# Performance work log

Hardware: AMD Instinct MI355X
Metric: run time of the kernel (lower is better)

The kernel has to match this reference:

```python
import jax, jax.numpy as jnp
import numpy as np
from jax.ops import segment_sum, segment_max

N, E, DS, DZ = 16384, 262144, 384, 128
H, D, PQ, PV = 12, 16, 4, 8
EPS = 1e-8


def _quat_to_rot(q):
    q = q / jnp.linalg.norm(q, axis=-1, keepdims=True)
    w, x, y, z = q[:, 0], q[:, 1], q[:, 2], q[:, 3]
    R = jnp.stack([
        1 - 2 * (y * y + z * z), 2 * (x * y - w * z), 2 * (x * z + w * y),
        2 * (x * y + w * z), 1 - 2 * (x * x + z * z), 2 * (y * z - w * x),
        2 * (x * z - w * y), 2 * (y * z + w * x), 1 - 2 * (x * x + y * y),
    ], axis=-1).reshape(-1, 3, 3)
    return R


def setup_inputs() -> dict:
    key = jax.random.key(0)
    ks = jax.random.split(key, 20)
    s = jax.random.normal(ks[0], (N, DS), jnp.float32)
    z = jax.random.normal(ks[1], (E, DZ), jnp.float32)
    edge_index = jax.random.randint(ks[2], (E, 2), 0, N, jnp.int64)
    # valid rigid frames: rotation from random unit quaternion + translation
    R = _quat_to_rot(jax.random.normal(ks[3], (N, 4), jnp.float32))
    t = jax.random.normal(ks[4], (N, 3), jnp.float32)
    f = jnp.zeros((N, 4, 4), jnp.float32).at[:, :3, :3].set(R)
    f = f.at[:, :3, 3].set(t).at[:, 3, 3].set(1.0)

    def lin(k, dout, din):
        return jax.random.normal(k, (dout, din), jnp.float32) / np.sqrt(din)

    hc, hpqk, hpv = H * D, H * PQ * 3, H * PV * 3
    s_out_dim = H * (D * 2 + PV * 4)
    params = dict(
        Wq=lin(ks[5], hc, DS), bq=jnp.zeros((hc,), jnp.float32),
        Wk=lin(ks[6], hc, DS), bk=jnp.zeros((hc,), jnp.float32),
        Wv=lin(ks[7], hc, DS), bv=jnp.zeros((hc,), jnp.float32),
        Wb=lin(ks[8], H, DZ), bb=jnp.zeros((H,), jnp.float32),
        Wqp=lin(ks[9], hpqk, DS), bqp=jnp.zeros((hpqk,), jnp.float32),
        Wkp=lin(ks[10], hpqk, DS), bkp=jnp.zeros((hpqk,), jnp.float32),
        Wvp=lin(ks[11], hpv, DS), bvp=jnp.zeros((hpv,), jnp.float32),
        head_weights=jnp.full((H,), 0.541324854612918, jnp.float32),
        Wpair=lin(ks[12], hc, DZ), bpair=jnp.zeros((hc,), jnp.float32),
        Wo=lin(ks[13], DS, s_out_dim), bo=jnp.zeros((DS,), jnp.float32),
    )
    return dict(s=s, z=z, f=f, edge_index=edge_index, **params)


def _ipa(s, z, f, edge_index, Wq, bq, Wk, bk, Wv, bv, Wb, bb,
         Wqp, bqp, Wkp, bkp, Wvp, bvp, head_weights, Wpair, bpair, Wo, bo):
    n = s.shape[0]
    R, t = f[:, :3, :3], f[:, :3, 3]
    idx_i, idx_j = edge_index[:, 0], edge_index[:, 1]

    norm_attn = (3.0 * D) ** 0.5          # (1/(3d))**-0.5 as in source
    norm_bias = 3.0 ** 0.5
    norm_pt = -0.5 * (3.0 * (PQ * 9.0 / 2)) ** 0.5

    q = (s @ Wq.T + bq).reshape(n, H, D)
    k = (s @ Wk.T + bk).reshape(n, H, D)
    v = (s @ Wv.T + bv).reshape(n, H, D)

    def to_global(pts):  # [n,H,P,3] local -> global
        return jnp.einsum('nij,nhpj->nhpi', R, pts) + t[:, None, None, :]

    q_pts = to_global((s @ Wqp.T + bqp).reshape(n, H, PQ, 3))
    k_pts = to_global((s @ Wkp.T + bkp).reshape(n, H, PQ, 3))
    v_pts = to_global((s @ Wvp.T + bvp).reshape(n, H, PV, 3))

    # scalar QK term + learned pair bias, per edge [E,H]
    attn = jnp.einsum('ehd,ehd->eh', q[idx_i], k[idx_j]) * norm_attn
    attn = attn + (z @ Wb.T + bb) * norm_bias
    # point-distance term
    diff = q_pts[idx_i] - k_pts[idx_j]            # [E,H,PQ,3]
    pt_att = (diff ** 2).sum((-1, -2))            # [E,H]
    pt_att = pt_att * (jax.nn.softplus(head_weights) * norm_pt)
    attn = attn + pt_att

    # segment softmax over edges grouped by destination node idx_i
    m = segment_max(attn, idx_i, num_segments=n)          # [N,H]
    ex = jnp.exp(attn - m[idx_i])
    denom = segment_sum(ex, idx_i, num_segments=n)
    a = ex / denom[idx_i]                                  # [E,H]

    o = segment_sum(a[:, :, None] * v[idx_j], idx_i, num_segments=n)  # [N,H,D]
    o = o.reshape(n, H * D)

    o_pts_g = segment_sum(a[:, :, None, None] * v_pts[idx_j], idx_i,
                          num_segments=n)                  # [N,H,PV,3]
    o_pts_g = o_pts_g.reshape(n, H * PV, 3)
    # invert_apply: R^T (p - t)
    o_pts = jnp.einsum('nji,npj->npi', R, o_pts_g - t[:, None, :])
    o_pts_norm = jnp.sqrt((o_pts ** 2).sum(-1) + EPS)      # [N,H*PV]
    o_pts_flat = o_pts.reshape(n, H * PV * 3)

    v_pair = (z @ Wpair.T + bpair).reshape(-1, H, D)       # [E,H,D]
    o_pair = segment_sum(a[:, :, None] * v_pair, idx_i, num_segments=n)
    o_pair = o_pair.reshape(n, H * D)

    o_s = jnp.concatenate([o, o_pts_flat, o_pts_norm, o_pair], axis=-1)
    return o_s @ Wo.T + bo


def reference(s, z, f, edge_index, Wq, bq, Wk, bk, Wv, bv, Wb, bb,
              Wqp, bqp, Wkp, bkp, Wvp, bvp, head_weights, Wpair, bpair, Wo, bo):
    s_out = _ipa(s, z, f, edge_index, Wq, bq, Wk, bk, Wv, bv, Wb, bb,
                 Wqp, bqp, Wkp, bkp, Wvp, bvp, head_weights, Wpair, bpair, Wo, bo)
    return (s_out, z)
```

## Files before the change

### kernel.cpp

```cpp
#include <hip/hip_runtime.h>

#define NNODE 16384
#define NEDGE 262144
#define DS    384
#define DZ    128
#define NH    12
#define HD    16
#define HC    192
#define HPQK  144
#define HPV   288
#define NCAT  1152
#define FEAT  2144
#define SOUT  384

typedef _Float16 f16;
typedef _Float16 f16x8 __attribute__((ext_vector_type(8)));
typedef _Float16 f16x4 __attribute__((ext_vector_type(4)));
typedef _Float16 f16x2 __attribute__((ext_vector_type(2)));
typedef float    f32x4v __attribute__((ext_vector_type(4)));

#define AS3(p) ((__attribute__((address_space(3))) void*)(p))
#define AS1(p) ((const __attribute__((address_space(1))) void*)(p))
#define WAVE_LDS_FENCE() asm volatile("s_waitcnt lgkmcnt(0)" ::: "memory")

__global__ void k_prep(const float* __restrict__ Wq, const float* __restrict__ Wk,
                       const float* __restrict__ Wv, const float* __restrict__ Wqp,
                       const float* __restrict__ Wkp, const float* __restrict__ Wvp,
                       const float* __restrict__ bq, const float* __restrict__ bk,
                       const float* __restrict__ bv, const float* __restrict__ bqp,
                       const float* __restrict__ bkp, const float* __restrict__ bvp,
                       const float* __restrict__ Wb, const float* __restrict__ Wo,
                       const float* __restrict__ Wpair, const float* __restrict__ bpair,
                       const float* __restrict__ hw,
                       f16* __restrict__ Wcat, float* __restrict__ bcat,
                       f16* __restrict__ Wb16, f16* __restrict__ M2,
                       float* __restrict__ gamv)
{
    int t = blockIdx.x * 256 + threadIdx.x;
    const int T0 = NCAT * DS;
    const int T1 = T0 + NCAT;
    const int T2 = T1 + 16 * DZ;
    const int T3 = T2 + SOUT * FEAT;
    const int T4 = T3 + NH;
    if (t < T0) {
        int r = t / DS, c = t - r * DS;
        float v;
        if      (r < 192) v = Wq [(r      ) * DS + c];
        else if (r < 384) v = Wk [(r - 192) * DS + c];
        else if (r < 576) v = Wv [(r - 384) * DS + c];
        else if (r < 720) v = Wqp[(r - 576) * DS + c];
        else if (r < 864) v = Wkp[(r - 720) * DS + c];
        else              v = Wvp[(r - 864) * DS + c];
        Wcat[t] = (f16)v;
    } else if (t < T1) {
        int r = t - T0;
        float v;
        if      (r < 192) v = bq [r];
        else if (r < 384) v = bk [r - 192];
        else if (r < 576) v = bv [r - 384];
        else if (r < 720) v = bqp[r - 576];
        else if (r < 864) v = bkp[r - 720];
        else              v = bvp[r - 864];
        bcat[r] = v;
    } else if (t < T2) {
        int q = t - T1;
        Wb16[q] = (q < NH * DZ) ? (f16)Wb[q] : (f16)0.0f;
    } else if (t < T3) {
        int q = t - T2;
        int r = q / FEAT, c = q - r * FEAT;
        float v = 0.f;
        if (c < 576) {
            v = Wo[r * 768 + c];
        } else if (c < 2112) {
            int h = (c - 576) >> 7, cc = (c - 576) & 127;
            float acc = 0.f;
            #pragma unroll
            for (int d = 0; d < 16; ++d)
                acc += Wo[r * 768 + 576 + h * 16 + d] * Wpair[(h * 16 + d) * DZ + cc];
            v = acc;
        } else if (c < 2124) {
            int h = c - 2112;
            float acc = 0.f;
            #pragma unroll
            for (int d = 0; d < 16; ++d)
                acc += Wo[r * 768 + 576 + h * 16 + d] * bpair[h * 16 + d];
            v = acc;
        }
        M2[q] = (f16)v;
    } else if (t < T4) {
        int h = t - T3;
        gamv[h] = -3.67423461f * log1pf(__expf(hw[h]));
    }
}

__global__ void k_convert_s(const float4* __restrict__ s4, f16* __restrict__ s16)
{
    int t = blockIdx.x * 256 + threadIdx.x;
    float4 v = s4[t];
    f16x4 o = { (f16)v.x, (f16)v.y, (f16)v.z, (f16)v.w };
    *(f16x4*)(s16 + 4 * (size_t)t) = o;
}

__global__ void k_zcopy(const float4* __restrict__ z4, f16* __restrict__ z16,
                        float4* __restrict__ zout4)
{
    int t = blockIdx.x * 256 + threadIdx.x;
    float4 v = z4[t];
    zout4[t] = v;
    f16x4 o = { (f16)v.x, (f16)v.y, (f16)v.z, (f16)v.w };
    *(f16x4*)(z16 + 4 * (size_t)t) = o;
}

__global__ __launch_bounds__(256) void k_zbias(const f16* __restrict__ z16,
                                               const f16* __restrict__ Wb16,
                                               const float* __restrict__ bb,
                                               float* __restrict__ zbias)
{
    const int wv = threadIdx.x >> 6, lane = threadIdx.x & 63;
    const int row0 = (blockIdx.x * 4 + wv) * 64;
    f16x8 bf[4];
    #pragma unroll
    for (int ks = 0; ks < 4; ++ks)
        bf[ks] = *(const f16x8*)(Wb16 + (lane & 15) * DZ + ks * 32 + (lane >> 4) * 8);
    #pragma unroll
    for (int tt = 0; tt < 4; ++tt) {
        int ra = row0 + tt * 16 + (lane & 15);
        f32x4v acc = {};
        #pragma unroll
        for (int ks = 0; ks < 4; ++ks) {
            f16x8 af = *(const f16x8*)(z16 + (size_t)ra * DZ + ks * 32 + (lane >> 4) * 8);
            acc = __builtin_amdgcn_mfma_f32_16x16x32_f16(af, bf[ks], acc, 0, 0, 0);
        }
        int col = lane & 15;
        if (col < NH) {
            #pragma unroll
            for (int r = 0; r < 4; ++r) {
                int row = row0 + tt * 16 + (lane >> 4) * 4 + r;
                zbias[(size_t)row * NH + col] = (acc[r] + bb[col]) * 1.73205081f;
            }
        }
    }
}

__global__ __launch_bounds__(256) void k_gemm(const f16* __restrict__ A, const f16* __restrict__ B,
                                              const float* __restrict__ bias, float* __restrict__ C,
                                              int M, int N, int K)
{
    __shared__ __align__(16) f16 As[128 * 32];
    __shared__ __align__(16) f16 Bs[128 * 32];
    const int tid = threadIdx.x;
    const int wave = tid >> 6, lane = tid & 63;
    const int bm = blockIdx.x, bn = blockIdx.y;
    const int wm = (wave >> 1) * 64, wn = (wave & 1) * 64;
    f32x4v acc[4][4] = {};
    const int srow = wave * 16 + (lane >> 2);
    const int scol = (lane & 3) * 8;
    const f16* gA0 = A + (size_t)(bm * 128 + srow) * K + scol;
    const f16* gA1 = A + (size_t)(bm * 128 + srow + 64) * K + scol;
    const f16* gB0 = B + (size_t)(bn * 128 + srow) * K + scol;
    const f16* gB1 = B + (size_t)(bn * 128 + srow + 64) * K + scol;
    f16* lA0 = As + wave * 512;
    f16* lA1 = As + (wave + 4) * 512;
    f16* lB0 = Bs + wave * 512;
    f16* lB1 = Bs + (wave + 4) * 512;
    const int fr = lane & 15, fc = (lane >> 4) * 8;
    const int nK = K >> 5;
    for (int kk = 0; kk < nK; ++kk) {
        __syncthreads();
        __builtin_amdgcn_global_load_lds(AS1(gA0), AS3(lA0), 16, 0, 0);
        __builtin_amdgcn_global_load_lds(AS1(gA1), AS3(lA1), 16, 0, 0);
        __builtin_amdgcn_global_load_lds(AS1(gB0), AS3(lB0), 16, 0, 0);
        __builtin_amdgcn_global_load_lds(AS1(gB1), AS3(lB1), 16, 0, 0);
        gA0 += 32; gA1 += 32; gB0 += 32; gB1 += 32;
        __syncthreads();
        f16x8 af[4], bf[4];
        #pragma unroll
        for (int mi = 0; mi < 4; ++mi)
            af[mi] = *(const f16x8*)(As + (wm + mi * 16 + fr) * 32 + fc);
        #pragma unroll
        for (int ni = 0; ni < 4; ++ni)
            bf[ni] = *(const f16x8*)(Bs + (wn + ni * 16 + fr) * 32 + fc);
        #pragma unroll
        for (int mi = 0; mi < 4; ++mi)
            #pragma unroll
            for (int ni = 0; ni < 4; ++ni)
                acc[mi][ni] = __builtin_amdgcn_mfma_f32_16x16x32_f16(af[mi], bf[ni], acc[mi][ni], 0, 0, 0);
    }
    const int r0 = bm * 128 + wm + (lane >> 4) * 4;
    const int c0 = bn * 128 + wn + (lane & 15);
    #pragma unroll
    for (int mi = 0; mi < 4; ++mi)
        #pragma unroll
        for (int ni = 0; ni < 4; ++ni) {
            int col = c0 + ni * 16;
            float b = bias[col];
            #pragma unroll
            for (int r = 0; r < 4; ++r) {
                int row = r0 + mi * 16 + r;
                C[(size_t)row * N + col] = acc[mi][ni][r] + b;
            }
        }
}

__global__ __launch_bounds__(256) void k_gemm16(const f16* __restrict__ A, const f16* __restrict__ B,
                                                const float* __restrict__ bias, f16* __restrict__ C,
                                                int M, int N, int K)
{
    __shared__ __align__(16) f16 As[128 * 32];
    __shared__ __align__(16) f16 Bs[128 * 32];
    const int tid = threadIdx.x;
    const int wave = tid >> 6, lane = tid & 63;
    const int bm = blockIdx.x, bn = blockIdx.y;
    const int wm = (wave >> 1) * 64, wn = (wave & 1) * 64;
    f32x4v acc[4][4] = {};
    const int srow = wave * 16 + (lane >> 2);
    const int scol = (lane & 3) * 8;
    const f16* gA0 = A + (size_t)(bm * 128 + srow) * K + scol;
    const f16* gA1 = A + (size_t)(bm * 128 + srow + 64) * K + scol;
    const f16* gB0 = B + (size_t)(bn * 128 + srow) * K + scol;
    const f16* gB1 = B + (size_t)(bn * 128 + srow + 64) * K + scol;
    f16* lA0 = As + wave * 512;
    f16* lA1 = As + (wave + 4) * 512;
    f16* lB0 = Bs + wave * 512;
    f16* lB1 = Bs + (wave + 4) * 512;
    const int fr = lane & 15, fc = (lane >> 4) * 8;
    const int nK = K >> 5;
    for (int kk = 0; kk < nK; ++kk) {
        __syncthreads();
        __builtin_amdgcn_global_load_lds(AS1(gA0), AS3(lA0), 16, 0, 0);
        __builtin_amdgcn_global_load_lds(AS1(gA1), AS3(lA1), 16, 0, 0);
        __builtin_amdgcn_global_load_lds(AS1(gB0), AS3(lB0), 16, 0, 0);
        __builtin_amdgcn_global_load_lds(AS1(gB1), AS3(lB1), 16, 0, 0);
        gA0 += 32; gA1 += 32; gB0 += 32; gB1 += 32;
        __syncthreads();
        f16x8 af[4], bf[4];
        #pragma unroll
        for (int mi = 0; mi < 4; ++mi)
            af[mi] = *(const f16x8*)(As + (wm + mi * 16 + fr) * 32 + fc);
        #pragma unroll
        for (int ni = 0; ni < 4; ++ni)
            bf[ni] = *(const f16x8*)(Bs + (wn + ni * 16 + fr) * 32 + fc);
        #pragma unroll
        for (int mi = 0; mi < 4; ++mi)
            #pragma unroll
            for (int ni = 0; ni < 4; ++ni)
                acc[mi][ni] = __builtin_amdgcn_mfma_f32_16x16x32_f16(af[mi], bf[ni], acc[mi][ni], 0, 0, 0);
    }
    const int r0 = bm * 128 + wm + (lane >> 4) * 4;
    const int c0 = bn * 128 + wn + (lane & 15);
    #pragma unroll
    for (int mi = 0; mi < 4; ++mi)
        #pragma unroll
        for (int ni = 0; ni < 4; ++ni) {
            int col = c0 + ni * 16;
            float b = bias[col];
            #pragma unroll
            for (int r = 0; r < 4; ++r) {
                int row = r0 + mi * 16 + r;
                C[(size_t)row * N + col] = (f16)(acc[mi][ni][r] + b);
            }
        }
}

__global__ __launch_bounds__(64) void k_nodepost(const f16* __restrict__ raw, const float* __restrict__ fmat,
        f16* __restrict__ Q16, f16* __restrict__ K16, f16* __restrict__ V16,
        f16* __restrict__ QP16, f16* __restrict__ KP16, f16* __restrict__ VP16)
{
    int n = blockIdx.x, l = threadIdx.x;
    const f16* r = raw + (size_t)n * NCAT;
    #pragma unroll
    for (int q = 0; q < 3; ++q) {
        int c = q * 64 + l;
        Q16[(size_t)n * HC + c] = r[c];
        K16[(size_t)n * HC + c] = r[HC + c];
        V16[(size_t)n * HC + c] = r[2 * HC + c];
    }
    const float* fp = fmat + (size_t)n * 16;
    float R00 = fp[0], R01 = fp[1], R02 = fp[2],  t0 = fp[3];
    float R10 = fp[4], R11 = fp[5], R12 = fp[6],  t1 = fp[7];
    float R20 = fp[8], R21 = fp[9], R22 = fp[10], t2 = fp[11];
    if (l < 48) {
        const f16* p = r + 576 + 3 * l;
        float x = (float)p[0], y = (float)p[1], zz = (float)p[2];
        QP16[(size_t)n * HPQK + 3 * l + 0] = (f16)(R00 * x + R01 * y + R02 * zz + t0);
        QP16[(size_t)n * HPQK + 3 * l + 1] = (f16)(R10 * x + R11 * y + R12 * zz + t1);
        QP16[(size_t)n * HPQK + 3 * l + 2] = (f16)(R20 * x + R21 * y + R22 * zz + t2);
        const f16* p2 = r + 720 + 3 * l;
        float x2 = (float)p2[0], y2 = (float)p2[1], z2 = (float)p2[2];
        KP16[(size_t)n * HPQK + 3 * l + 0] = (f16)(R00 * x2 + R01 * y2 + R02 * z2 + t0);
        KP16[(size_t)n * HPQK + 3 * l + 1] = (f16)(R10 * x2 + R11 * y2 + R12 * z2 + t1);
        KP16[(size_t)n * HPQK + 3 * l + 2] = (f16)(R20 * x2 + R21 * y2 + R22 * z2 + t2);
    }
    {
        const f16* p = r + 864 + 3 * l;
        float x = (float)p[0], y = (float)p[1], zz = (float)p[2];
        VP16[(size_t)n * HPV + 3 * l + 0] = (f16)(R00 * x + R01 * y + R02 * zz + t0);
        VP16[(size_t)n * HPV + 3 * l + 1] = (f16)(R10 * x + R11 * y + R12 * zz + t1);
        VP16[(size_t)n * HPV + 3 * l + 2] = (f16)(R20 * x + R21 * y + R22 * zz + t2);
    }
    if (l < 32) {
        int tt = 64 + l;
        const f16* p = r + 864 + 3 * tt;
        float x = (float)p[0], y = (float)p[1], zz = (float)p[2];
        VP16[(size_t)n * HPV + 3 * tt + 0] = (f16)(R00 * x + R01 * y + R02 * zz + t0);
        VP16[(size_t)n * HPV + 3 * tt + 1] = (f16)(R10 * x + R11 * y + R12 * zz + t1);
        VP16[(size_t)n * HPV + 3 * tt + 2] = (f16)(R20 * x + R21 * y + R22 * zz + t2);
    }
}

__global__ void k_zero(int* counts, int* cursor) {
    int t = blockIdx.x * 256 + threadIdx.x;
    if (t < NNODE) counts[t] = 0;
    else if (t < 2 * NNODE) cursor[t - NNODE] = 0;
}
__global__ void k_count(const int* __restrict__ ei, int* counts) {
    int e = blockIdx.x * 256 + threadIdx.x;
    if (e < NEDGE) atomicAdd(&counts[ei[2 * e]], 1);
}
__global__ void k_scan(const int* __restrict__ counts, int* __restrict__ rowptr) {
    __shared__ int lds[256];
    int t = threadIdx.x;
    const int per = NNODE / 256;
    int s = 0;
    for (int i = 0; i < per; ++i) s += counts[t * per + i];
    lds[t] = s; __syncthreads();
    for (int off = 1; off < 256; off <<= 1) {
        int v = (t >= off) ? lds[t - off] : 0;
        __syncthreads();
        lds[t] += v;
        __syncthreads();
    }
    int run = (t == 0) ? 0 : lds[t - 1];
    for (int i = 0; i < per; ++i) { rowptr[t * per + i] = run; run += counts[t * per + i]; }
    if (t == 255) rowptr[NNODE] = run;
}
__global__ void k_scatter(const int* __restrict__ ei, const int* __restrict__ rowptr,
                          int* cursor, int* __restrict__ eids, int* __restrict__ jsorted,
                          int* __restrict__ isorted) {
    int e = blockIdx.x * 256 + threadIdx.x;
    if (e < NEDGE) {
        int i = ei[2 * e];
        int pos = rowptr[i] + atomicAdd(&cursor[i], 1);
        eids[pos] = e;
        jsorted[pos] = ei[2 * e + 1];
        isorted[pos] = i;
    }
}

__global__ __launch_bounds__(256) void k_logits2(
    const int* __restrict__ eids,
    const int* __restrict__ isorted, const int* __restrict__ jsorted,
    const float* __restrict__ zbias,
    const f16* __restrict__ Q16, const f16* __restrict__ K16,
    const f16* __restrict__ QP16, const f16* __restrict__ KP16,
    const float* __restrict__ gamv, float* __restrict__ attn)
{
    const int pos = blockIdx.x * 256 + threadIdx.x;
    const int i = isorted[pos], j = jsorted[pos];
    const int e = eids[pos];
    const f16x8* qr = (const f16x8*)(Q16 + (size_t)i * HC);
    const f16x8* kr = (const f16x8*)(K16 + (size_t)j * HC);
    const f16* qpp = QP16 + (size_t)i * HPQK;
    const f16* kpp = KP16 + (size_t)j * HPQK;
    const float4* zbp = (const float4*)(zbias + (size_t)e * NH);
    float4 zb0 = zbp[0], zb1 = zbp[1], zb2 = zbp[2];
    float zb[NH] = { zb0.x, zb0.y, zb0.z, zb0.w, zb1.x, zb1.y, zb1.z, zb1.w,
                     zb2.x, zb2.y, zb2.z, zb2.w };
    float out[NH];
    #pragma unroll
    for (int h = 0; h < NH; ++h) {
        f16x8 q0 = qr[2 * h], q1 = qr[2 * h + 1];
        f16x8 k0 = kr[2 * h], k1 = kr[2 * h + 1];
        float d = 0.f;
        #pragma unroll
        for (int u = 0; u < 8; ++u)
            d += (float)q0[u] * (float)k0[u] + (float)q1[u] * (float)k1[u];
        float pt = 0.f;
        #pragma unroll
        for (int c = 0; c < 3; ++c) {
            f16x4 qpc = *(const f16x4*)(qpp + 12 * h + 4 * c);
            f16x4 kpc = *(const f16x4*)(kpp + 12 * h + 4 * c);
            #pragma unroll
            for (int u = 0; u < 4; ++u) {
                float dd = (float)qpc[u] - (float)kpc[u];
                pt += dd * dd;
            }
        }
        out[h] = 6.92820323f * d + zb[h] + gamv[h] * pt;
    }
    float4* ao = (float4*)(attn + (size_t)pos * NH);
    ao[0] = make_float4(out[0], out[1], out[2], out[3]);
    ao[1] = make_float4(out[4], out[5], out[6], out[7]);
    ao[2] = make_float4(out[8], out[9], out[10], out[11]);
}

__global__ __launch_bounds__(256) void k_soft(
    const int* __restrict__ rowptr, const float* __restrict__ attn,
    f16* __restrict__ a16, f16* __restrict__ feat)
{
    const int lane = threadIdx.x & 63, wv = threadIdx.x >> 6;
    const int slot = lane >> 4, el = lane & 15;
    const int n = blockIdx.x * 16 + wv * 4 + slot;
    const int base = rowptr[n], deg = rowptr[n + 1] - base;

    f16* fo = feat + (size_t)n * FEAT;
    fo[2112 + el]      = (f16)((el < NH && deg > 0) ? 1.0f : 0.0f);
    fo[2112 + 16 + el] = (f16)0.0f;

    float lg[NH];
    if (deg <= 16) {
        if (el < deg) {
            const float4* ar = (const float4*)(attn + (size_t)(base + el) * NH);
            float4 a0 = ar[0], a1 = ar[1], a2 = ar[2];
            lg[0]=a0.x; lg[1]=a0.y; lg[2]=a0.z; lg[3]=a0.w;
            lg[4]=a1.x; lg[5]=a1.y; lg[6]=a1.z; lg[7]=a1.w;
            lg[8]=a2.x; lg[9]=a2.y; lg[10]=a2.z; lg[11]=a2.w;
        } else {
            #pragma unroll
            for (int h = 0; h < NH; ++h) lg[h] = -1e30f;
        }
        #pragma unroll
        for (int h = 0; h < NH; ++h) {
            float v = lg[h];
            v = fmaxf(v, __shfl_xor(v, 1));
            v = fmaxf(v, __shfl_xor(v, 2));
            v = fmaxf(v, __shfl_xor(v, 4));
            v = fmaxf(v, __shfl_xor(v, 8));
            float e = __expf(lg[h] - v);
            float ssum = e;
            ssum += __shfl_xor(ssum, 1);
            ssum += __shfl_xor(ssum, 2);
            ssum += __shfl_xor(ssum, 4);
            ssum += __shfl_xor(ssum, 8);
            lg[h] = (ssum > 0.f) ? e / ssum : 0.f;
        }
        if (el < deg) {
            f16x8 o0, o1;
            #pragma unroll
            for (int h = 0; h < 8; ++h) o0[h] = (f16)lg[h];
            #pragma unroll
            for (int h = 8; h < 12; ++h) o1[h - 8] = (f16)lg[h];
            o1[4] = o1[5] = o1[6] = o1[7] = (f16)0.0f;
            f16* ap = a16 + (size_t)(base + el) * 16;
            *(f16x8*)ap = o0;
            *(f16x8*)(ap + 8) = o1;
        }
    } else {
        const int nch = (deg + 15) >> 4;
        float mx[NH];
        #pragma unroll
        for (int h = 0; h < NH; ++h) mx[h] = -1e30f;
        for (int c = 0; c < nch; ++c) {
            int idx = c * 16 + el;
            if (idx < deg) {
                const float4* ar = (const float4*)(attn + (size_t)(base + idx) * NH);
                float4 a0 = ar[0], a1 = ar[1], a2 = ar[2];
                float v[NH] = { a0.x,a0.y,a0.z,a0.w, a1.x,a1.y,a1.z,a1.w, a2.x,a2.y,a2.z,a2.w };
                #pragma unroll
                for (int h = 0; h < NH; ++h) mx[h] = fmaxf(mx[h], v[h]);
            }
        }
        #pragma unroll
        for (int h = 0; h < NH; ++h) {
            float v = mx[h];
            v = fmaxf(v, __shfl_xor(v, 1));
            v = fmaxf(v, __shfl_xor(v, 2));
            v = fmaxf(v, __shfl_xor(v, 4));
            v = fmaxf(v, __shfl_xor(v, 8));
            mx[h] = v;
        }
        float ls[NH] = {};
        for (int c = 0; c < nch; ++c) {
            int idx = c * 16 + el;
            if (idx < deg) {
                const float4* ar = (const float4*)(attn + (size_t)(base + idx) * NH);
                float4 a0 = ar[0], a1 = ar[1], a2 = ar[2];
                float v[NH] = { a0.x,a0.y,a0.z,a0.w, a1.x,a1.y,a1.z,a1.w, a2.x,a2.y,a2.z,a2.w };
                f16x8 o0, o1;
                #pragma unroll
                for (int h = 0; h < NH; ++h) {
                    float e = __expf(v[h] - mx[h]);
                    ls[h] += e;
                    if (h < 8) o0[h] = (f16)e; else o1[h - 8] = (f16)e;
                }
                o1[4] = o1[5] = o1[6] = o1[7] = (f16)0.0f;
                f16* ap = a16 + (size_t)(base + idx) * 16;
                *(f16x8*)ap = o0;
                *(f16x8*)(ap + 8) = o1;
            }
        }
        float il[NH];
        #pragma unroll
        for (int h = 0; h < NH; ++h) {
            float v = ls[h];
            v += __shfl_xor(v, 1);
            v += __shfl_xor(v, 2);
            v += __shfl_xor(v, 4);
            v += __shfl_xor(v, 8);
            il[h] = (v > 0.f) ? 1.0f / v : 0.f;
        }
        for (int c = 0; c < nch; ++c) {
            int idx = c * 16 + el;
            if (idx < deg) {
                f16* ap = a16 + (size_t)(base + idx) * 16;
                f16x8 o0 = *(f16x8*)ap;
                f16x8 o1 = *(f16x8*)(ap + 8);
                #pragma unroll
                for (int h = 0; h < 8; ++h) o0[h] = (f16)((float)o0[h] * il[h]);
                #pragma unroll
                for (int h = 8; h < 12; ++h) o1[h - 8] = (f16)((float)o1[h - 8] * il[h]);
                *(f16x8*)ap = o0;
                *(f16x8*)(ap + 8) = o1;
            }
        }
    }
}

__global__ __launch_bounds__(256) void k_aggu(
    const int* __restrict__ rowptr, const int* __restrict__ eids,
    const f16* __restrict__ a16, const f16* __restrict__ z16, f16* __restrict__ feat)
{
    __shared__ f16 ash[4][64 * 16];
    __shared__ int esh[4][64];
    const int wv = threadIdx.x >> 6, lane = threadIdx.x & 63;
    const int n = blockIdx.x * 4 + wv;
    const int base = rowptr[n], deg = rowptr[n + 1] - base;
    float u0[NH] = {}, u1[NH] = {};
    const int nch = (deg + 63) >> 6;
    for (int c = 0; c < nch; ++c) {
        int cl = min(64, deg - c * 64);
        if (lane < cl) {
            size_t pos = (size_t)(base + c * 64 + lane);
            const f16x8* ap = (const f16x8*)(a16 + pos * 16);
            *(f16x8*)&ash[wv][lane * 16] = ap[0];
            *(f16x8*)&ash[wv][lane * 16 + 8] = ap[1];
            esh[wv][lane] = eids[pos];
        }
        WAVE_LDS_FENCE();
        for (int kk = 0; kk < cl; ++kk) {
            int e = esh[wv][kk];
            f16x2 zv = *(const f16x2*)(z16 + (size_t)e * DZ + 2 * lane);
            float z0 = (float)zv[0], z1 = (float)zv[1];
            #pragma unroll
            for (int i = 0; i < 6; ++i) {
                f16x2 a2 = *(const f16x2*)&ash[wv][kk * 16 + 2 * i];
                float a0 = (float)a2[0], a1 = (float)a2[1];
                u0[2 * i]     += a0 * z0; u1[2 * i]     += a0 * z1;
                u0[2 * i + 1] += a1 * z0; u1[2 * i + 1] += a1 * z1;
            }
        }
        WAVE_LDS_FENCE();
    }
    f16* fo = feat + (size_t)n * FEAT + 576;
    #pragma unroll
    for (int h = 0; h < NH; ++h) {
        f16x2 o = { (f16)u0[h], (f16)u1[h] };
        *(f16x2*)(fo + h * DZ + 2 * lane) = o;
    }
}

__global__ __launch_bounds__(256) void k_aggv(
    const int* __restrict__ rowptr, const int* __restrict__ jsorted,
    const f16* __restrict__ a16, const f16* __restrict__ V16,
    const f16* __restrict__ VP16, const float* __restrict__ fmat,
    f16* __restrict__ feat)
{
    __shared__ f16 ash[4][64 * 16];
    __shared__ int jsh[4][64];
    __shared__ float psh[2][HPV];
    const int w4 = threadIdx.x >> 6;
    const int lane = threadIdx.x & 63;
    const int slot = w4 >> 1;
    const int role = w4 & 1;
    const int n = blockIdx.x * 2 + slot;
    const int base = rowptr[n], deg = rowptr[n + 1] - base;
    const int nch = (deg + 63) >> 6;

    float o0 = 0, o1 = 0, o2 = 0;
    const int hA = lane >> 4, hB = (64 + lane) >> 4, hC2 = (128 + lane) >> 4;
    float acc[5] = {};
    int hk[5];
    #pragma unroll
    for (int k = 0; k < 5; ++k) hk[k] = (k * 64 + lane) / 24;

    for (int c = 0; c < nch; ++c) {
        int cl = min(64, deg - c * 64);
        if (lane < cl) {
            size_t pos = (size_t)(base + c * 64 + lane);
            const f16x8* ap = (const f16x8*)(a16 + pos * 16);
            *(f16x8*)&ash[w4][lane * 16] = ap[0];
            *(f16x8*)&ash[w4][lane * 16 + 8] = ap[1];
            jsh[w4][lane] = jsorted[pos];
        }
        WAVE_LDS_FENCE();
        if (role == 0) {
            for (int kk = 0; kk < cl; ++kk) {
                int j = jsh[w4][kk];
                const f16* vr = V16 + (size_t)j * HC;
                float aA = (float)ash[w4][kk * 16 + hA];
                float aB = (float)ash[w4][kk * 16 + hB];
                float aC = (float)ash[w4][kk * 16 + hC2];
                o0 += aA * (float)vr[lane];
                o1 += aB * (float)vr[64 + lane];
                o2 += aC * (float)vr[128 + lane];
            }
        } else {
            for (int kk = 0; kk < cl; ++kk) {
                int j = jsh[w4][kk];
                const f16* vp = VP16 + (size_t)j * HPV;
                #pragma unroll
                for (int k = 0; k < 4; ++k)
                    acc[k] += (float)ash[w4][kk * 16 + hk[k]] * (float)vp[k * 64 + lane];
                if (lane < 32)
                    acc[4] += (float)ash[w4][kk * 16 + hk[4]] * (float)vp[256 + lane];
            }
        }
        WAVE_LDS_FENCE();
    }

    f16* fo = feat + (size_t)n * FEAT;
    if (role == 0) {
        fo[lane] = (f16)o0; fo[64 + lane] = (f16)o1; fo[128 + lane] = (f16)o2;
    } else {
        #pragma unroll
        for (int k = 0; k < 4; ++k) psh[slot][k * 64 + lane] = acc[k];
        if (lane < 32) psh[slot][256 + lane] = acc[4];
        WAVE_LDS_FENCE();
        const float* fp = fmat + (size_t)n * 16;
        float R00 = fp[0], R01 = fp[1], R02 = fp[2],  t0 = fp[3];
        float R10 = fp[4], R11 = fp[5], R12 = fp[6],  t1 = fp[7];
        float R20 = fp[8], R21 = fp[9], R22 = fp[10], t2 = fp[11];
        {
            int P = lane;
            float gx = psh[slot][3 * P] - t0, gy = psh[slot][3 * P + 1] - t1, gz = psh[slot][3 * P + 2] - t2;
            float lx = R00 * gx + R10 * gy + R20 * gz;
            float ly = R01 * gx + R11 * gy + R21 * gz;
            float lz = R02 * gx + R12 * gy + R22 * gz;
            fo[192 + 3 * P] = (f16)lx; fo[192 + 3 * P + 1] = (f16)ly; fo[192 + 3 * P + 2] = (f16)lz;
            fo[480 + P] = (f16)sqrtf(lx * lx + ly * ly + lz * lz + 1e-8f);
        }
        if (lane < 32) {
            int P = 64 + lane;
            float gx = psh[slot][3 * P] - t0, gy = psh[slot][3 * P + 1] - t1, gz = psh[slot][3 * P + 2] - t2;
            float lx = R00 * gx + R10 * gy + R20 * gz;
            float ly = R01 * gx + R11 * gy + R21 * gz;
            float lz = R02 * gx + R12 * gy + R22 * gz;
            fo[192 + 3 * P] = (f16)lx; fo[192 + 3 * P + 1] = (f16)ly; fo[192 + 3 * P + 2] = (f16)lz;
            fo[480 + P] = (f16)sqrtf(lx * lx + ly * ly + lz * lz + 1e-8f);
        }
    }
}

extern "C" void kernel_launch(void* const* d_in, const int* in_sizes, int n_in,
                              void* d_out, int out_size, void* d_ws, size_t ws_size,
                              hipStream_t stream)
{
    (void)in_sizes; (void)n_in; (void)out_size; (void)ws_size;
    const float* s     = (const float*)d_in[0];
    const float* z     = (const float*)d_in[1];
    const float* fmat  = (const float*)d_in[2];
    const int*   ei    = (const int*)d_in[3];
    const float* Wq    = (const float*)d_in[4];
    const float* bq    = (const float*)d_in[5];
    const float* Wk    = (const float*)d_in[6];
    const float* bk    = (const float*)d_in[7];
    const float* Wv    = (const float*)d_in[8];
    const float* bv    = (const float*)d_in[9];
    const float* Wb    = (const float*)d_in[10];
    const float* bb    = (const float*)d_in[11];
    const float* Wqp   = (const float*)d_in[12];
    const float* bqp   = (const float*)d_in[13];
    const float* Wkp   = (const float*)d_in[14];
    const float* bkp   = (const float*)d_in[15];
    const float* Wvp   = (const float*)d_in[16];
    const float* bvp   = (const float*)d_in[17];
    const float* hw    = (const float*)d_in[18];
    const float* Wpair = (const float*)d_in[19];
    const float* bpair = (const float*)d_in[20];
    const float* Wo    = (const float*)d_in[21];
    const float* bo    = (const float*)d_in[22];

    char* w = (char*)d_ws;
    auto alloc = [&](size_t bytes) { char* p = w; w += (bytes + 255) & ~(size_t)255; return p; };
    f16*   s16     = (f16*)  alloc((size_t)NNODE * DS * 2);
    f16*   Wcat    = (f16*)  alloc((size_t)NCAT * DS * 2);
    float* bcat    = (float*)alloc((size_t)NCAT * 4);
    f16*   Wb16    = (f16*)  alloc((size_t)16 * DZ * 2);
    f16*   M2      = (f16*)  alloc((size_t)SOUT * FEAT * 2);
    float* gamv    = (float*)alloc((size_t)NH * 4);
    int*   counts  = (int*)  alloc((size_t)NNODE * 4);
    int*   rowptr  = (int*)  alloc((size_t)(NNODE + 1) * 4);
    int*   cursor  = (int*)  alloc((size_t)NNODE * 4);
    int*   eids    = (int*)  alloc((size_t)NEDGE * 4);
    int*   jsorted = (int*)  alloc((size_t)NEDGE * 4);
    int*   isorted = (int*)  alloc((size_t)NEDGE * 4);
    float* attn    = (float*)alloc((size_t)NEDGE * NH * 4);
    f16*   z16     = (f16*)  alloc((size_t)NEDGE * DZ * 2);
    float* zbias   = (float*)alloc((size_t)NEDGE * NH * 4);
    f16*   Q16     = (f16*)  alloc((size_t)NNODE * HC * 2);
    f16*   K16     = (f16*)  alloc((size_t)NNODE * HC * 2);
    f16*   QP16    = (f16*)  alloc((size_t)NNODE * HPQK * 2);
    f16*   KP16    = (f16*)  alloc((size_t)NNODE * HPQK * 2);
    f16*   V16     = (f16*)  alloc((size_t)NNODE * HC * 2);
    f16*   VP16    = (f16*)  alloc((size_t)NNODE * HPV * 2);
    f16*   a16     = (f16*)  alloc((size_t)NEDGE * 16 * 2);
    char*  U       = w;
    f16*   raw16   = (f16*)U;
    f16*   feat    = (f16*)U;

    float* zout = (float*)d_out + (size_t)NNODE * DS;

    const int PREP_T = NCAT * DS + NCAT + 16 * DZ + SOUT * FEAT + NH;
    k_prep<<<(PREP_T + 255) / 256, 256, 0, stream>>>(Wq, Wk, Wv, Wqp, Wkp, Wvp,
        bq, bk, bv, bqp, bkp, bvp, Wb, Wo, Wpair, bpair, hw, Wcat, bcat, Wb16, M2, gamv);
    k_zero<<<(2 * NNODE) / 256, 256, 0, stream>>>(counts, cursor);
    k_count<<<NEDGE / 256, 256, 0, stream>>>(ei, counts);
    k_scan<<<1, 256, 0, stream>>>(counts, rowptr);
    k_scatter<<<NEDGE / 256, 256, 0, stream>>>(ei, rowptr, cursor, eids, jsorted, isorted);
    k_convert_s<<<(NNODE * DS / 4) / 256, 256, 0, stream>>>((const float4*)s, s16);
    k_zcopy<<<(NEDGE * DZ / 4) / 256, 256, 0, stream>>>((const float4*)z, z16, (float4*)zout);
    k_zbias<<<NEDGE / 256, 256, 0, stream>>>(z16, Wb16, bb, zbias);
    k_gemm16<<<dim3(NNODE / 128, NCAT / 128), 256, 0, stream>>>(s16, Wcat, bcat, raw16,
        NNODE, NCAT, DS);
    k_nodepost<<<NNODE, 64, 0, stream>>>(raw16, fmat, Q16, K16, V16, QP16, KP16, VP16);
    k_logits2<<<NEDGE / 256, 256, 0, stream>>>(eids, isorted, jsorted, zbias, Q16, K16,
        QP16, KP16, gamv, attn);
    k_soft<<<NNODE / 16, 256, 0, stream>>>(rowptr, attn, a16, feat);
    k_aggu<<<NNODE / 4, 256, 0, stream>>>(rowptr, eids, a16, z16, feat);
    k_aggv<<<NNODE / 2, 256, 0, stream>>>(rowptr, jsorted, a16, V16, VP16, fmat, feat);
    k_gemm<<<dim3(NNODE / 128, SOUT / 128), 256, 0, stream>>>(feat, M2, bo, (float*)d_out,
        NNODE, SOUT, FEAT);
}
```

Before: 404.8 us.

## Read Q/K/V directly from projection output and widen output GEMM N-tile

Result: slower. 416.8 us (+3.0%).

```diff
diff --git a/kernel.cpp b/kernel.cpp
--- a/kernel.cpp
+++ b/kernel.cpp
@@ -142,9 +142,9 @@
     }
 }
 
-__global__ __launch_bounds__(256) void k_gemm(const f16* __restrict__ A, const f16* __restrict__ B,
-                                              const float* __restrict__ bias, float* __restrict__ C,
-                                              int M, int N, int K)
+__global__ __launch_bounds__(256) void k_gemm16(const f16* __restrict__ A, const f16* __restrict__ B,
+                                                const float* __restrict__ bias, f16* __restrict__ C,
+                                                int M, int N, int K)
 {
     __shared__ __align__(16) f16 As[128 * 32];
     __shared__ __align__(16) f16 Bs[128 * 32];
@@ -197,32 +197,34 @@
             #pragma unroll
             for (int r = 0; r < 4; ++r) {
                 int row = r0 + mi * 16 + r;
-                C[(size_t)row * N + col] = acc[mi][ni][r] + b;
-            }
-        }
-}
-
-__global__ __launch_bounds__(256) void k_gemm16(const f16* __restrict__ A, const f16* __restrict__ B,
-                                                const float* __restrict__ bias, f16* __restrict__ C,
-                                                int M, int N, int K)
+                C[(size_t)row * N + col] = (f16)(acc[mi][ni][r] + b);
+            }
+        }
+}
+
+__global__ __launch_bounds__(256) void k_gemm_out(const f16* __restrict__ A, const f16* __restrict__ B,
+                                                  const float* __restrict__ bias, float* __restrict__ C,
+                                                  int M, int N, int K)
 {
     __shared__ __align__(16) f16 As[128 * 32];
-    __shared__ __align__(16) f16 Bs[128 * 32];
+    __shared__ __align__(16) f16 Bs[192 * 32];
     const int tid = threadIdx.x;
     const int wave = tid >> 6, lane = tid & 63;
     const int bm = blockIdx.x, bn = blockIdx.y;
-    const int wm = (wave >> 1) * 64, wn = (wave & 1) * 64;
-    f32x4v acc[4][4] = {};
-    const int srow = wave * 16 + (lane >> 2);
+    const int wm = (wave >> 1) * 64, wn = (wave & 1) * 96;
+    f32x4v acc[4][6] = {};
+    const int lrow = lane >> 2;
     const int scol = (lane & 3) * 8;
-    const f16* gA0 = A + (size_t)(bm * 128 + srow) * K + scol;
-    const f16* gA1 = A + (size_t)(bm * 128 + srow + 64) * K + scol;
-    const f16* gB0 = B + (size_t)(bn * 128 + srow) * K + scol;
-    const f16* gB1 = B + (size_t)(bn * 128 + srow + 64) * K + scol;
-    f16* lA0 = As + wave * 512;
-    f16* lA1 = As + (wave + 4) * 512;
-    f16* lB0 = Bs + wave * 512;
-    f16* lB1 = Bs + (wave + 4) * 512;
+    const f16* gA0 = A + (size_t)(bm * 128 + wave * 16 + lrow) * K + scol;
+    const f16* gA1 = A + (size_t)(bm * 128 + 64 + wave * 16 + lrow) * K + scol;
+    f16* lA0 = As + (wave * 16) * 32;
+    f16* lA1 = As + (64 + wave * 16) * 32;
+    const f16* gB0 = B + (size_t)(bn * 192 + wave * 48 + lrow) * K + scol;
+    const f16* gB1 = B + (size_t)(bn * 192 + wave * 48 + 16 + lrow) * K + scol;
+    const f16* gB2 = B + (size_t)(bn * 192 + wave * 48 + 32 + lrow) * K + scol;
+    f16* lB0 = Bs + (wave * 48) * 32;
+    f16* lB1 = Bs + (wave * 48 + 16) * 32;
+    f16* lB2 = Bs + (wave * 48 + 32) * 32;
     const int fr = lane & 15, fc = (lane >> 4) * 8;
     const int nK = K >> 5;
     for (int kk = 0; kk < nK; ++kk) {
@@ -231,50 +233,43 @@
         __builtin_amdgcn_global_load_lds(AS1(gA1), AS3(lA1), 16, 0, 0);
         __builtin_amdgcn_global_load_lds(AS1(gB0), AS3(lB0), 16, 0, 0);
         __builtin_amdgcn_global_load_lds(AS1(gB1), AS3(lB1), 16, 0, 0);
-        gA0 += 32; gA1 += 32; gB0 += 32; gB1 += 32;
+        __builtin_amdgcn_global_load_lds(AS1(gB2), AS3(lB2), 16, 0, 0);
+        gA0 += 32; gA1 += 32; gB0 += 32; gB1 += 32; gB2 += 32;
         __syncthreads();
-        f16x8 af[4], bf[4];
+        f16x8 af[4], bf[6];
         #pragma unroll
         for (int mi = 0; mi < 4; ++mi)
             af[mi] = *(const f16x8*)(As + (wm + mi * 16 + fr) * 32 + fc);
         #pragma unroll
-        for (int ni = 0; ni < 4; ++ni)
+        for (int ni = 0; ni < 6; ++ni)
             bf[ni] = *(const f16x8*)(Bs + (wn + ni * 16 + fr) * 32 + fc);
         #pragma unroll
         for (int mi = 0; mi < 4; ++mi)
             #pragma unroll
-            for (int ni = 0; ni < 4; ++ni)
+            for (int ni = 0; ni < 6; ++ni)
                 acc[mi][ni] = __builtin_amdgcn_mfma_f32_16x16x32_f16(af[mi], bf[ni], acc[mi][ni], 0, 0, 0);
     }
     const int r0 = bm * 128 + wm + (lane >> 4) * 4;
-    const int c0 = bn * 128 + wn + (lane & 15);
+    const int c0 = bn * 192 + wn + (lane & 15);
     #pragma unroll
     for (int mi = 0; mi < 4; ++mi)
         #pragma unroll
-        for (int ni = 0; ni < 4; ++ni) {
+        for (int ni = 0; ni < 6; ++ni) {
             int col = c0 + ni * 16;
             float b = bias[col];
             #pragma unroll
             for (int r = 0; r < 4; ++r) {
                 int row = r0 + mi * 16 + r;
-                C[(size_t)row * N + col] = (f16)(acc[mi][ni][r] + b);
+                C[(size_t)row * N + col] = acc[mi][ni][r] + b;
             }
         }
 }
 
 __global__ __launch_bounds__(64) void k_nodepost(const f16* __restrict__ raw, const float* __restrict__ fmat,
-        f16* __restrict__ Q16, f16* __restrict__ K16, f16* __restrict__ V16,
         f16* __restrict__ QP16, f16* __restrict__ KP16, f16* __restrict__ VP16)
 {
     int n = blockIdx.x, l = threadIdx.x;
     const f16* r = raw + (size_t)n * NCAT;
-    #pragma unroll
-    for (int q = 0; q < 3; ++q) {
-        int c = q * 64 + l;
-        Q16[(size_t)n * HC + c] = r[c];
-        K16[(size_t)n * HC + c] = r[HC + c];
-        V16[(size_t)n * HC + c] = r[2 * HC + c];
-    }
     const float* fp = fmat + (size_t)n * 16;
     float R00 = fp[0], R01 = fp[1], R02 = fp[2],  t0 = fp[3];
     float R10 = fp[4], R11 = fp[5], R12 = fp[6],  t1 = fp[7];
@@ -350,16 +345,15 @@
 __global__ __launch_bounds__(256) void k_logits2(
     const int* __restrict__ eids,
     const int* __restrict__ isorted, const int* __restrict__ jsorted,
-    const float* __restrict__ zbias,
-    const f16* __restrict__ Q16, const f16* __restrict__ K16,
+    const float* __restrict__ zbias, const f16* __restrict__ raw,
     const f16* __restrict__ QP16, const f16* __restrict__ KP16,
     const float* __restrict__ gamv, float* __restrict__ attn)
 {
     const int pos = blockIdx.x * 256 + threadIdx.x;
     const int i = isorted[pos], j = jsorted[pos];
     const int e = eids[pos];
-    const f16x8* qr = (const f16x8*)(Q16 + (size_t)i * HC);
-    const f16x8* kr = (const f16x8*)(K16 + (size_t)j * HC);
+    const f16x8* qr = (const f16x8*)(raw + (size_t)i * NCAT);
+    const f16x8* kr = (const f16x8*)(raw + (size_t)j * NCAT + HC);
     const f16* qpp = QP16 + (size_t)i * HPQK;
     const f16* kpp = KP16 + (size_t)j * HPQK;
     const float4* zbp = (const float4*)(zbias + (size_t)e * NH);
@@ -561,7 +555,7 @@
 
 __global__ __launch_bounds__(256) void k_aggv(
     const int* __restrict__ rowptr, const int* __restrict__ jsorted,
-    const f16* __restrict__ a16, const f16* __restrict__ V16,
+    const f16* __restrict__ a16, const f16* __restrict__ raw,
     const f16* __restrict__ VP16, const float* __restrict__ fmat,
     f16* __restrict__ feat)
 {
@@ -596,7 +590,7 @@
         if (role == 0) {
             for (int kk = 0; kk < cl; ++kk) {
                 int j = jsh[w4][kk];
-                const f16* vr = V16 + (size_t)j * HC;
+                const f16* vr = raw + (size_t)j * NCAT + 2 * HC;
                 float aA = (float)ash[w4][kk * 16 + hA];
                 float aB = (float)ash[w4][kk * 16 + hB];
                 float aC = (float)ash[w4][kk * 16 + hC2];
@@ -697,16 +691,12 @@
     float* attn    = (float*)alloc((size_t)NEDGE * NH * 4);
     f16*   z16     = (f16*)  alloc((size_t)NEDGE * DZ * 2);
     float* zbias   = (float*)alloc((size_t)NEDGE * NH * 4);
-    f16*   Q16     = (f16*)  alloc((size_t)NNODE * HC * 2);
-    f16*   K16     = (f16*)  alloc((size_t)NNODE * HC * 2);
     f16*   QP16    = (f16*)  alloc((size_t)NNODE * HPQK * 2);
     f16*   KP16    = (f16*)  alloc((size_t)NNODE * HPQK * 2);
-    f16*   V16     = (f16*)  alloc((size_t)NNODE * HC * 2);
     f16*   VP16    = (f16*)  alloc((size_t)NNODE * HPV * 2);
     f16*   a16     = (f16*)  alloc((size_t)NEDGE * 16 * 2);
-    char*  U       = w;
-    f16*   raw16   = (f16*)U;
-    f16*   feat    = (f16*)U;
+    f16*   raw16   = (f16*)  alloc((size_t)NNODE * NCAT * 2);
+    f16*   feat    = (f16*)  alloc((size_t)NNODE * FEAT * 2);
 
     float* zout = (float*)d_out + (size_t)NNODE * DS;
 
@@ -722,12 +712,12 @@
     k_zbias<<<NEDGE / 256, 256, 0, stream>>>(z16, Wb16, bb, zbias);
     k_gemm16<<<dim3(NNODE / 128, NCAT / 128), 256, 0, stream>>>(s16, Wcat, bcat, raw16,
         NNODE, NCAT, DS);
-    k_nodepost<<<NNODE, 64, 0, stream>>>(raw16, fmat, Q16, K16, V16, QP16, KP16, VP16);
-    k_logits2<<<NEDGE / 256, 256, 0, stream>>>(eids, isorted, jsorted, zbias, Q16, K16,
+    k_nodepost<<<NNODE, 64, 0, stream>>>(raw16, fmat, QP16, KP16, VP16);
+    k_logits2<<<NEDGE / 256, 256, 0, stream>>>(eids, isorted, jsorted, zbias, raw16,
         QP16, KP16, gamv, attn);
     k_soft<<<NNODE / 16, 256, 0, stream>>>(rowptr, attn, a16, feat);
     k_aggu<<<NNODE / 4, 256, 0, stream>>>(rowptr, eids, a16, z16, feat);
-    k_aggv<<<NNODE / 2, 256, 0, stream>>>(rowptr, jsorted, a16, V16, VP16, fmat, feat);
-    k_gemm<<<dim3(NNODE / 128, SOUT / 128), 256, 0, stream>>>(feat, M2, bo, (float*)d_out,
+    k_aggv<<<NNODE / 2, 256, 0, stream>>>(rowptr, jsorted, a16, raw16, VP16, fmat, feat);
+    k_gemm_out<<<dim3(NNODE / 128, SOUT / 192), 256, 0, stream>>>(feat, M2, bo, (float*)d_out,
         NNODE, SOUT, FEAT);
 }
```
